# Optimization experiments

Measured on AMD Instinct MI355X. Metric: run time of the kernel, lower is better.

## Reference

```python
import jax, jax.numpy as jnp
import numpy as np


def _mlp2(x, w1, b1, w2, b2):
    # Linear -> LeakyReLU(0.01, torch default) -> Linear
    return jax.nn.leaky_relu(x @ w1 + b1) @ w2 + b2


def _fuse(vis, phr):
    # pairwise fusion: concat[vis, phr, vis*phr, vis-phr] -> last dim 4*R
    shp = jnp.broadcast_shapes(vis.shape, phr.shape)
    v = jnp.broadcast_to(vis, shp)
    p = jnp.broadcast_to(phr, shp)
    return jnp.concatenate([v, p, v * p, v - p], axis=-1)


def setup_inputs() -> dict:
    key = jax.random.key(0)
    B, P, N, D, R = 4, 16, 256, 2048, 1024
    ks = jax.random.split(key, 16)
    w = lambda k, s: jax.random.normal(k, s, jnp.float32) * 0.02
    inp = {
        "box_feats": jax.random.normal(ks[0], (B, N, D), jnp.float32),
        "phrase_embed": jax.random.normal(ks[1], (B, P, R), jnp.float32),
        # visual_embedding MLP (stage 1)
        "ve_w1": w(ks[2], (D, R)), "ve_b1": jnp.zeros((R,), jnp.float32),
        "ve_w2": w(ks[3], (R, R)), "ve_b2": jnp.zeros((R,), jnp.float32),
        # similarity MLP: 4R -> 256 -> 1
        "sim_w1": w(ks[4], (4 * R, 256)), "sim_b1": jnp.zeros((256,), jnp.float32),
        "sim_w2": w(ks[5], (256, 1)), "sim_b2": jnp.zeros((1,), jnp.float32),
        # box_reg MLP: 4R -> 256 -> 4
        "reg_w1": w(ks[6], (4 * R, 256)), "reg_b1": jnp.zeros((256,), jnp.float32),
        "reg_w2": w(ks[7], (256, 4)), "reg_b2": jnp.zeros((4,), jnp.float32),
        # topN-stage twins
        "vet_w1": w(ks[8], (D, R)), "vet_b1": jnp.zeros((R,), jnp.float32),
        "vet_w2": w(ks[9], (R, R)), "vet_b2": jnp.zeros((R,), jnp.float32),
        "simt_w1": w(ks[10], (4 * R, 256)), "simt_b1": jnp.zeros((256,), jnp.float32),
        "simt_w2": w(ks[11], (256, 1)), "simt_b2": jnp.zeros((1,), jnp.float32),
        "regt_w1": w(ks[12], (4 * R, 256)), "regt_b1": jnp.zeros((256,), jnp.float32),
        "regt_w2": w(ks[13], (256, 4)), "regt_b2": jnp.zeros((4,), jnp.float32),
        "topN": 16,
    }
    return inp


def reference(box_feats, phrase_embed,
              ve_w1, ve_b1, ve_w2, ve_b2,
              sim_w1, sim_b1, sim_w2, sim_b2,
              reg_w1, reg_b1, reg_w2, reg_b2,
              vet_w1, vet_b1, vet_w2, vet_b2,
              simt_w1, simt_b1, simt_w2, simt_b2,
              regt_w1, regt_b1, regt_w2, regt_b2,
              topN):
    # Stage 1: embed all boxes, score every (phrase, box) pair.
    vis = _mlp2(box_feats, ve_w1, ve_b1, ve_w2, ve_b2)          # [B,N,R]
    fused = _fuse(vis[:, None], phrase_embed[:, :, None])        # [B,P,N,4R]
    sim = jax.nn.softmax(
        _mlp2(fused, sim_w1, sim_b1, sim_w2, sim_b2)[..., 0], axis=-1)  # [B,P,N]
    reg = _mlp2(fused, reg_w1, reg_b1, reg_w2, reg_b2)           # [B,P,N,4]

    # Stage 2: topN rescoring per phrase (make_pair_topN pattern).
    _, top_idx = jax.lax.top_k(sim, topN)                        # [B,P,topN]
    bf_top = jnp.take_along_axis(box_feats[:, None], top_idx[..., None], axis=2)  # [B,P,topN,D]
    vis_t = _mlp2(bf_top, vet_w1, vet_b1, vet_w2, vet_b2)        # [B,P,topN,R]
    fused_t = _fuse(vis_t, phrase_embed[:, :, None])             # [B,P,topN,4R]
    sim_t = jax.nn.softmax(
        _mlp2(fused_t, simt_w1, simt_b1, simt_w2, simt_b2)[..., 0], axis=-1)  # [B,P,topN]
    reg_t = _mlp2(fused_t, regt_w1, regt_b1, regt_w2, regt_b2)   # [B,P,topN,4]
    return (sim, reg, sim_t, reg_t)
```

## Files before the change

kernel.cpp:

```cpp
#include <hip/hip_runtime.h>
#include <hip/hip_bf16.h>


namespace {

constexpr int Nc_   = 256;
constexpr int Dc    = 2048;
constexpr int Rc    = 1024;
constexpr int TOPN  = 16;
constexpr int HS    = 256;
constexpr int HO    = 512;
constexpr int BPc   = 64;
constexpr int PAIRS1 = 16384;
constexpr int PAIRS2 = 1024;

__device__ __forceinline__ float  leaky01f(float x)  { return x > 0.f ? x : 0.01f * x; }
__device__ __forceinline__ double leaky01d(double x) { return x > 0.0 ? x : 0.01  * x; }

template <typename TA, typename TW, bool ST64, bool ST32, bool LEAKY>
__global__ __launch_bounds__(256) void dgemm64_kernel(
    const TA* __restrict__ A, const TW* __restrict__ W, const float* __restrict__ bias,
    double* __restrict__ C64, float* __restrict__ C32, int M, int N, int K)
{
  __shared__ double As[16][64];
  __shared__ double Bs[16][64];
  const int t = threadIdx.x, tx = t & 15, ty = t >> 4;
  const int row0 = blockIdx.y * 64, col0 = blockIdx.x * 64;
  double acc[4][4] = {};

  for (int k0 = 0; k0 < K; k0 += 16) {
    {
      int mm = t >> 2, kq = (t & 3) * 4;
      const TA* src = A + (size_t)(row0 + mm) * K + k0 + kq;
      double v0, v1, v2, v3;
      if constexpr (sizeof(TA) == 4) {
        float4 f = *(const float4*)src; v0 = f.x; v1 = f.y; v2 = f.z; v3 = f.w;
      } else {
        const double2* d = (const double2*)src;
        double2 a = d[0], b = d[1]; v0 = a.x; v1 = a.y; v2 = b.x; v3 = b.y;
      }
      As[kq + 0][mm] = v0; As[kq + 1][mm] = v1; As[kq + 2][mm] = v2; As[kq + 3][mm] = v3;
    }
    {
      int kk = t >> 4, nq = (t & 15) * 4;
      const TW* src = W + (size_t)(k0 + kk) * N + col0 + nq;
      if constexpr (sizeof(TW) == 4) {
        float4 f = *(const float4*)src;
        Bs[kk][nq] = f.x; Bs[kk][nq + 1] = f.y; Bs[kk][nq + 2] = f.z; Bs[kk][nq + 3] = f.w;
      } else {
        const double2* d = (const double2*)src;
        double2 a = d[0], b = d[1];
        Bs[kk][nq] = a.x; Bs[kk][nq + 1] = a.y; Bs[kk][nq + 2] = b.x; Bs[kk][nq + 3] = b.y;
      }
    }
    __syncthreads();
#pragma unroll
    for (int kk = 0; kk < 16; ++kk) {
      double a[4], b[4];
#pragma unroll
      for (int i = 0; i < 4; ++i) a[i] = As[kk][ty * 4 + i];
#pragma unroll
      for (int j = 0; j < 4; ++j) b[j] = Bs[kk][tx * 4 + j];
#pragma unroll
      for (int i = 0; i < 4; ++i)
#pragma unroll
        for (int j = 0; j < 4; ++j) acc[i][j] = fma(a[i], b[j], acc[i][j]);
    }
    __syncthreads();
  }

#pragma unroll
  for (int i = 0; i < 4; ++i) {
    int r = row0 + ty * 4 + i;
#pragma unroll
    for (int j = 0; j < 4; ++j) {
      int c = col0 + tx * 4 + j;
      double v = acc[i][j];
      if (bias) v += (double)bias[c];
      if constexpr (LEAKY) v = leaky01d(v);
      if constexpr (ST64) C64[(size_t)r * N + c] = v;
      if constexpr (ST32) C32[(size_t)r * N + c] = (float)v;
    }
  }
}

__global__ __launch_bounds__(256) void pair64_kernel(
    const double* __restrict__ vis, const float* __restrict__ phr,
    const double* __restrict__ W, const double* __restrict__ Xv,
    const double* __restrict__ Xp, const double* __restrict__ b1,
    double* __restrict__ H)
{
  __shared__ double As[16][64];
  __shared__ double Bs[16][64];
  const int t = threadIdx.x, tx = t & 15, ty = t >> 4;
  const int row0 = blockIdx.y * 64, col0 = blockIdx.x * 64;
  double acc[4][4] = {};

  for (int k0 = 0; k0 < Rc; k0 += 16) {
    {
      int mm = t >> 2, kq = (t & 3) * 4;
      int m = row0 + mm, bp = m >> 8;
      int vr = ((bp >> 4) << 8) | (m & 255), pr = bp;
      const double2* vd = (const double2*)(vis + (size_t)vr * Rc + k0 + kq);
      double2 a = vd[0], b = vd[1];
      float4 p = *(const float4*)(phr + (size_t)pr * Rc + k0 + kq);
      As[kq + 0][mm] = a.x * (double)p.x; As[kq + 1][mm] = a.y * (double)p.y;
      As[kq + 2][mm] = b.x * (double)p.z; As[kq + 3][mm] = b.y * (double)p.w;
    }
    {
      int kk = t >> 4, nq = (t & 15) * 4;
      const double2* d = (const double2*)(W + (size_t)(k0 + kk) * HS + col0 + nq);
      double2 a = d[0], b = d[1];
      Bs[kk][nq] = a.x; Bs[kk][nq + 1] = a.y; Bs[kk][nq + 2] = b.x; Bs[kk][nq + 3] = b.y;
    }
    __syncthreads();
#pragma unroll
    for (int kk = 0; kk < 16; ++kk) {
      double a[4], b[4];
#pragma unroll
      for (int i = 0; i < 4; ++i) a[i] = As[kk][ty * 4 + i];
#pragma unroll
      for (int j = 0; j < 4; ++j) b[j] = Bs[kk][tx * 4 + j];
#pragma unroll
      for (int i = 0; i < 4; ++i)
#pragma unroll
        for (int j = 0; j < 4; ++j) acc[i][j] = fma(a[i], b[j], acc[i][j]);
    }
    __syncthreads();
  }

#pragma unroll
  for (int i = 0; i < 4; ++i) {
    int r = row0 + ty * 4 + i, bp = r >> 8;
    int vr = ((bp >> 4) << 8) | (r & 255), pr = bp;
#pragma unroll
    for (int j = 0; j < 4; ++j) {
      int c = col0 + tx * 4 + j;
      double v = acc[i][j] + Xv[(size_t)vr * HS + c] + Xp[(size_t)pr * HS + c] + b1[c];
      H[(size_t)r * HS + c] = leaky01d(v);
    }
  }
}

template <int BM, int BN, int BK, int TM, int TN>
__global__ __launch_bounds__(256) void sgemm_kernel(
    const float* __restrict__ A, const float* __restrict__ W,
    const float* __restrict__ bias, float* __restrict__ C,
    int M, int Nc, int K, int leaky)
{
  constexpr int THREADS = (BM / TM) * (BN / TN);
  static_assert(THREADS == 256, "block must be 256");
  __shared__ float As[BK][BM];
  __shared__ float Bs[BK][BN];

  const int t = threadIdx.x;
  const int tx = t % (BN / TN), ty = t / (BN / TN);
  const int row0 = blockIdx.y * BM, col0 = blockIdx.x * BN;
  float acc[TM][TN] = {};

  for (int k0 = 0; k0 < K; k0 += BK) {
    constexpr int AV = BM * BK / 4 / THREADS;
#pragma unroll
    for (int p_ = 0; p_ < AV; ++p_) {
      int f = p_ * THREADS + t;
      int mm = f / (BK / 4), kq = (f % (BK / 4)) * 4;
      float4 a4 = *(const float4*)(A + (size_t)(row0 + mm) * K + k0 + kq);
      As[kq + 0][mm] = a4.x; As[kq + 1][mm] = a4.y;
      As[kq + 2][mm] = a4.z; As[kq + 3][mm] = a4.w;
    }
    constexpr int BV = BK * BN / 4 / THREADS;
#pragma unroll
    for (int p_ = 0; p_ < BV; ++p_) {
      int f = p_ * THREADS + t;
      int nq = (f % (BN / 4)) * 4, kk = f / (BN / 4);
      *(float4*)&Bs[kk][nq] = *(const float4*)(W + (size_t)(k0 + kk) * Nc + col0 + nq);
    }
    __syncthreads();
#pragma unroll
    for (int kk = 0; kk < BK; ++kk) {
      float a[TM], bb[TN];
#pragma unroll
      for (int i = 0; i < TM; i += 4) {
        float4 v = *(const float4*)&As[kk][ty * TM + i];
        a[i] = v.x; a[i + 1] = v.y; a[i + 2] = v.z; a[i + 3] = v.w;
      }
#pragma unroll
      for (int j = 0; j < TN; j += 4) {
        float4 v = *(const float4*)&Bs[kk][tx * TN + j];
        bb[j] = v.x; bb[j + 1] = v.y; bb[j + 2] = v.z; bb[j + 3] = v.w;
      }
#pragma unroll
      for (int i = 0; i < TM; ++i)
#pragma unroll
        for (int j = 0; j < TN; ++j) acc[i][j] = fmaf(a[i], bb[j], acc[i][j]);
    }
    __syncthreads();
  }

#pragma unroll
  for (int i = 0; i < TM; ++i) {
    int r = row0 + ty * TM + i;
#pragma unroll
    for (int j = 0; j < TN; j += 4) {
      int c = col0 + tx * TN + j;
      float4 o;
      o.x = acc[i][j]; o.y = acc[i][j + 1]; o.z = acc[i][j + 2]; o.w = acc[i][j + 3];
      if (bias) {
        float4 bv = *(const float4*)(bias + c);
        o.x += bv.x; o.y += bv.y; o.z += bv.z; o.w += bv.w;
      }
      if (leaky) { o.x = leaky01f(o.x); o.y = leaky01f(o.y); o.z = leaky01f(o.z); o.w = leaky01f(o.w); }
      *(float4*)(C + (size_t)r * Nc + c) = o;
    }
  }
}

template <int BM, int BN, int BK, int TM, int TN, int STAGE, int NCOL, typename TVIS>
__global__ __launch_bounds__(256) void pair_gemm_kernel(
    const TVIS* __restrict__ vis, const float* __restrict__ phr,
    const float* __restrict__ Wvp, const float* __restrict__ Xv,
    const float* __restrict__ Xp, const float* __restrict__ b1c,
    float* __restrict__ Hout, int M)
{
  constexpr int THREADS = (BM / TM) * (BN / TN);
  static_assert(THREADS == 256, "block must be 256");
  __shared__ float As[BK][BM];
  __shared__ float Bs[BK][BN];

  const int t = threadIdx.x;
  const int tx = t % (BN / TN), ty = t / (BN / TN);
  const int row0 = blockIdx.y * BM, col0 = blockIdx.x * BN;
  float acc[TM][TN] = {};

  for (int k0 = 0; k0 < Rc; k0 += BK) {
    constexpr int AV = BM * BK / 4 / THREADS;
#pragma unroll
    for (int p_ = 0; p_ < AV; ++p_) {
      int f = p_ * THREADS + t;
      int mm = f / (BK / 4), kq = (f % (BK / 4)) * 4;
      int m = row0 + mm;
      int vr, pr;
      if (STAGE == 1) { int bp = m >> 8; pr = bp; vr = ((bp >> 4) << 8) | (m & 255); }
      else            { vr = m; pr = m >> 4; }
      float4 v4;
      if constexpr (sizeof(TVIS) == 8) {
        const double2* d = (const double2*)(vis + (size_t)vr * Rc + k0 + kq);
        double2 a = d[0], b = d[1];
        v4 = make_float4((float)a.x, (float)a.y, (float)b.x, (float)b.y);
      } else {
        v4 = *(const float4*)((const float*)vis + (size_t)vr * Rc + k0 + kq);
      }
      float4 p4 = *(const float4*)(phr + (size_t)pr * Rc + k0 + kq);
      As[kq + 0][mm] = v4.x * p4.x; As[kq + 1][mm] = v4.y * p4.y;
      As[kq + 2][mm] = v4.z * p4.z; As[kq + 3][mm] = v4.w * p4.w;
    }
    constexpr int BV = BK * BN / 4 / THREADS;
#pragma unroll
    for (int p_ = 0; p_ < BV; ++p_) {
      int f = p_ * THREADS + t;
      int nq = (f % (BN / 4)) * 4, kk = f / (BN / 4);
      *(float4*)&Bs[kk][nq] = *(const float4*)(Wvp + (size_t)(k0 + kk) * NCOL + col0 + nq);
    }
    __syncthreads();
#pragma unroll
    for (int kk = 0; kk < BK; ++kk) {
      float a[TM], bb[TN];
#pragma unroll
      for (int i = 0; i < TM; i += 4) {
        float4 v = *(const float4*)&As[kk][ty * TM + i];
        a[i] = v.x; a[i + 1] = v.y; a[i + 2] = v.z; a[i + 3] = v.w;
      }
#pragma unroll
      for (int j = 0; j < TN; j += 4) {
        float4 v = *(const float4*)&Bs[kk][tx * TN + j];
        bb[j] = v.x; bb[j + 1] = v.y; bb[j + 2] = v.z; bb[j + 3] = v.w;
      }
#pragma unroll
      for (int i = 0; i < TM; ++i)
#pragma unroll
        for (int j = 0; j < TN; ++j) acc[i][j] = fmaf(a[i], bb[j], acc[i][j]);
    }
    __syncthreads();
  }

#pragma unroll
  for (int i = 0; i < TM; ++i) {
    int r = row0 + ty * TM + i;
    int vr, pr;
    if (STAGE == 1) { int bp = r >> 8; pr = bp; vr = ((bp >> 4) << 8) | (r & 255); }
    else            { vr = r; pr = r >> 4; }
#pragma unroll
    for (int j = 0; j < TN; j += 4) {
      int c = col0 + tx * TN + j;
      float4 xv = *(const float4*)(Xv + (size_t)vr * NCOL + c);
      float4 xp = *(const float4*)(Xp + (size_t)pr * NCOL + c);
      float4 bv = *(const float4*)(b1c + c);
      float4 o;
      o.x = leaky01f(acc[i][j]     + xv.x + xp.x + bv.x);
      o.y = leaky01f(acc[i][j + 1] + xv.y + xp.y + bv.y);
      o.z = leaky01f(acc[i][j + 2] + xv.z + xp.z + bv.z);
      o.w = leaky01f(acc[i][j + 3] + xv.w + xp.w + bv.w);
      *(float4*)(Hout + (size_t)r * NCOL + c) = o;
    }
  }
}

__global__ __launch_bounds__(256) void prep_sim64_kernel(
    const float* __restrict__ w1, const float* __restrict__ b1,
    double* __restrict__ Wv, double* __restrict__ Wp, double* __restrict__ Wvp,
    double* __restrict__ bO)
{
  int idx = blockIdx.x * 256 + threadIdx.x;
  int r = idx >> 8, c = idx & 255;
  double wa = (double)w1[(size_t)(0 * Rc + r) * 256 + c];
  double wb = (double)w1[(size_t)(1 * Rc + r) * 256 + c];
  double wc = (double)w1[(size_t)(2 * Rc + r) * 256 + c];
  double wd = (double)w1[(size_t)(3 * Rc + r) * 256 + c];
  Wv[idx] = wa + wd; Wp[idx] = wb - wd; Wvp[idx] = wc;
  if (r == 0) bO[c] = (double)b1[c];
}

__global__ __launch_bounds__(256) void prep_reg32_kernel(
    const float* __restrict__ w1, const float* __restrict__ b1,
    float* __restrict__ Wv, float* __restrict__ Wp, float* __restrict__ Wvp,
    float* __restrict__ bO)
{
  int idx = blockIdx.x * 256 + threadIdx.x;
  int r = idx >> 8, c = idx & 255;
  float wa = w1[(size_t)(0 * Rc + r) * 256 + c];
  float wb = w1[(size_t)(1 * Rc + r) * 256 + c];
  float wc = w1[(size_t)(2 * Rc + r) * 256 + c];
  float wd = w1[(size_t)(3 * Rc + r) * 256 + c];
  Wv[idx] = wa + wd; Wp[idx] = wb - wd; Wvp[idx] = wc;
  if (r == 0) bO[c] = b1[c];
}

__global__ __launch_bounds__(256) void prep_t_kernel(
    const float* __restrict__ simw1, const float* __restrict__ regw1,
    const float* __restrict__ simb1, const float* __restrict__ regb1,
    float* __restrict__ Wv, float* __restrict__ Wp, float* __restrict__ Wvp,
    float* __restrict__ b1c)
{
  int idx = blockIdx.x * 256 + threadIdx.x;
  int r = idx >> 9, j = idx & (HO - 1);
  const float* w1 = (j < 256) ? simw1 : regw1;
  int c = j & 255;
  float wa = w1[(size_t)(0 * Rc + r) * 256 + c];
  float wb = w1[(size_t)(1 * Rc + r) * 256 + c];
  float wc = w1[(size_t)(2 * Rc + r) * 256 + c];
  float wd = w1[(size_t)(3 * Rc + r) * 256 + c];
  Wv[idx] = wa + wd; Wp[idx] = wb - wd; Wvp[idx] = wc;
  if (r == 0) b1c[j] = (j < 256) ? simb1[c] : regb1[c];
}

__global__ __launch_bounds__(256) void layer2_sim64_kernel(
    const double* __restrict__ h, const float* __restrict__ sw2,
    const float* __restrict__ sb2, double* __restrict__ out, int M)
{
  int wave = (blockIdx.x * blockDim.x + threadIdx.x) >> 6, lane = threadIdx.x & 63;
  if (wave >= M) return;
  const double* hr = h + (size_t)wave * HS + lane * 4;
  double2 h0 = *(const double2*)hr, h1 = *(const double2*)(hr + 2);
  float4 w = *(const float4*)(sw2 + lane * 4);
  double s = h0.x * (double)w.x + h0.y * (double)w.y + h1.x * (double)w.z + h1.y * (double)w.w;
#pragma unroll
  for (int off = 32; off; off >>= 1) s += __shfl_xor(s, off);
  if (lane == 0) out[wave] = s + (double)sb2[0];
}

__global__ __launch_bounds__(256) void layer2_reg32_kernel(
    const float* __restrict__ h, const float* __restrict__ rw2,
    const float* __restrict__ rb2, float* __restrict__ reg_out, int M)
{
  int wave = (blockIdx.x * blockDim.x + threadIdx.x) >> 6, lane = threadIdx.x & 63;
  if (wave >= M) return;
  float4 hr = *(const float4*)(h + (size_t)wave * HS + lane * 4);
  float4 r0 = *(const float4*)(rw2 + (size_t)(lane * 4 + 0) * 4);
  float4 r1 = *(const float4*)(rw2 + (size_t)(lane * 4 + 1) * 4);
  float4 r2 = *(const float4*)(rw2 + (size_t)(lane * 4 + 2) * 4);
  float4 r3 = *(const float4*)(rw2 + (size_t)(lane * 4 + 3) * 4);
  float c0 = hr.x * r0.x + hr.y * r1.x + hr.z * r2.x + hr.w * r3.x;
  float c1 = hr.x * r0.y + hr.y * r1.y + hr.z * r2.y + hr.w * r3.y;
  float c2 = hr.x * r0.z + hr.y * r1.z + hr.z * r2.z + hr.w * r3.z;
  float c3 = hr.x * r0.w + hr.y * r1.w + hr.z * r2.w + hr.w * r3.w;
#pragma unroll
  for (int off = 32; off; off >>= 1) {
    c0 += __shfl_xor(c0, off); c1 += __shfl_xor(c1, off);
    c2 += __shfl_xor(c2, off); c3 += __shfl_xor(c3, off);
  }
  if (lane == 0) {
    float4 o; o.x = c0 + rb2[0]; o.y = c1 + rb2[1]; o.z = c2 + rb2[2]; o.w = c3 + rb2[3];
    *(float4*)(reg_out + (size_t)wave * 4) = o;
  }
}

__global__ __launch_bounds__(256) void layer2_t_kernel(
    const float* __restrict__ hidden,
    const float* __restrict__ sw2, const float* __restrict__ sb2,
    const float* __restrict__ rw2, const float* __restrict__ rb2,
    float* __restrict__ sim_logits, float* __restrict__ reg_out, int M)
{
  int wave = (blockIdx.x * blockDim.x + threadIdx.x) >> 6, lane = threadIdx.x & 63;
  if (wave >= M) return;
  const float* h = hidden + (size_t)wave * HO;
  float4 hs = *(const float4*)(h + lane * 4);
  float4 hr = *(const float4*)(h + 256 + lane * 4);
  float4 ws = *(const float4*)(sw2 + lane * 4);
  float s = hs.x * ws.x + hs.y * ws.y + hs.z * ws.z + hs.w * ws.w;
  float4 r0 = *(const float4*)(rw2 + (size_t)(lane * 4 + 0) * 4);
  float4 r1 = *(const float4*)(rw2 + (size_t)(lane * 4 + 1) * 4);
  float4 r2 = *(const float4*)(rw2 + (size_t)(lane * 4 + 2) * 4);
  float4 r3 = *(const float4*)(rw2 + (size_t)(lane * 4 + 3) * 4);
  float c0 = hr.x * r0.x + hr.y * r1.x + hr.z * r2.x + hr.w * r3.x;
  float c1 = hr.x * r0.y + hr.y * r1.y + hr.z * r2.y + hr.w * r3.y;
  float c2 = hr.x * r0.z + hr.y * r1.z + hr.z * r2.z + hr.w * r3.z;
  float c3 = hr.x * r0.w + hr.y * r1.w + hr.z * r2.w + hr.w * r3.w;
#pragma unroll
  for (int off = 32; off; off >>= 1) {
    s  += __shfl_xor(s, off);
    c0 += __shfl_xor(c0, off); c1 += __shfl_xor(c1, off);
    c2 += __shfl_xor(c2, off); c3 += __shfl_xor(c3, off);
  }
  if (lane == 0) {
    sim_logits[wave] = s + sb2[0];
    float4 o; o.x = c0 + rb2[0]; o.y = c1 + rb2[1]; o.z = c2 + rb2[2]; o.w = c3 + rb2[3];
    *(float4*)(reg_out + (size_t)wave * 4) = o;
  }
}

__global__ __launch_bounds__(64) void softmax_topk64_kernel(
    const double* __restrict__ logits, float* __restrict__ sim_out,
    int* __restrict__ top_idx)
{
  int row = blockIdx.x, lane = threadIdx.x;
  double v[4];
#pragma unroll
  for (int i = 0; i < 4; ++i) v[i] = logits[row * 256 + i * 64 + lane];
  double m = fmax(fmax(v[0], v[1]), fmax(v[2], v[3]));
#pragma unroll
  for (int off = 32; off; off >>= 1) m = fmax(m, __shfl_xor(m, off));
  double e[4], ssum = 0.0;
#pragma unroll
  for (int i = 0; i < 4; ++i) { e[i] = exp(v[i] - m); ssum += e[i]; }
#pragma unroll
  for (int off = 32; off; off >>= 1) ssum += __shfl_xor(ssum, off);
#pragma unroll
  for (int i = 0; i < 4; ++i)
    sim_out[row * 256 + i * 64 + lane] = (float)(e[i] / ssum);

  const double EPS = 2.5e-7;
  for (int it = 0; it < TOPN; ++it) {
    double vm = fmax(fmax(v[0], v[1]), fmax(v[2], v[3]));
#pragma unroll
    for (int off = 32; off; off >>= 1) vm = fmax(vm, __shfl_xor(vm, off));
    double thr = vm - EPS;
    int bi = 1 << 30;
#pragma unroll
    for (int i = 0; i < 4; ++i)
      if (v[i] >= thr) { int gi = i * 64 + lane; if (gi < bi) bi = gi; }
#pragma unroll
    for (int off = 32; off; off >>= 1) {
      int oi = __shfl_xor(bi, off);
      if (oi < bi) bi = oi;
    }
    if (lane == 0) top_idx[row * TOPN + it] = bi;
    if ((bi & 63) == lane) v[bi >> 6] = -1.0e30;
  }
}

__global__ __launch_bounds__(64) void softmax16_kernel(
    const float* __restrict__ logits, float* __restrict__ out)
{
  int row = blockIdx.x, lane = threadIdx.x;
  float v = (lane < TOPN) ? logits[row * TOPN + lane] : -1e30f;
  float m = v;
#pragma unroll
  for (int off = 8; off; off >>= 1) m = fmaxf(m, __shfl_xor(m, off));
  float e = (lane < TOPN) ? expf(v - m) : 0.f;
  float s = e;
#pragma unroll
  for (int off = 8; off; off >>= 1) s += __shfl_xor(s, off);
  if (lane < TOPN) out[row * TOPN + lane] = e / s;
}

__global__ __launch_bounds__(256) void gather_kernel(
    const float* __restrict__ box, const int* __restrict__ top_idx,
    float* __restrict__ bf_top)
{
  int pr = blockIdx.x;
  int bp = pr >> 4, b = bp >> 4;
  int src = b * Nc_ + top_idx[pr];
  const float4* s = (const float4*)(box + (size_t)src * Dc);
  float4* d = (float4*)(bf_top + (size_t)pr * Dc);
  for (int i = threadIdx.x; i < Dc / 4; i += 256) d[i] = s[i];
}

}

extern "C" void kernel_launch(void* const* d_in, const int* in_sizes, int n_in,
                              void* d_out, int out_size, void* d_ws, size_t ws_size,
                              hipStream_t stream) {
  const float* box    = (const float*)d_in[0];
  const float* phrase = (const float*)d_in[1];
  const float* ve_w1  = (const float*)d_in[2];
  const float* ve_b1  = (const float*)d_in[3];
  const float* ve_w2  = (const float*)d_in[4];
  const float* ve_b2  = (const float*)d_in[5];
  const float* sim_w1 = (const float*)d_in[6];
  const float* sim_b1 = (const float*)d_in[7];
  const float* sim_w2 = (const float*)d_in[8];
  const float* sim_b2 = (const float*)d_in[9];
  const float* reg_w1 = (const float*)d_in[10];
  const float* reg_b1 = (const float*)d_in[11];
  const float* reg_w2 = (const float*)d_in[12];
  const float* reg_b2 = (const float*)d_in[13];
  const float* vet_w1 = (const float*)d_in[14];
  const float* vet_b1 = (const float*)d_in[15];
  const float* vet_w2 = (const float*)d_in[16];
  const float* vet_b2 = (const float*)d_in[17];
  const float* simt_w1 = (const float*)d_in[18];
  const float* simt_b1 = (const float*)d_in[19];
  const float* simt_w2 = (const float*)d_in[20];
  const float* simt_b2 = (const float*)d_in[21];
  const float* regt_w1 = (const float*)d_in[22];
  const float* regt_b1 = (const float*)d_in[23];
  const float* regt_w2 = (const float*)d_in[24];
  const float* regt_b2 = (const float*)d_in[25];

  float* out = (float*)d_out;
  float* o_sim  = out;
  float* o_reg  = out + PAIRS1;
  float* o_simt = out + 81920;
  float* o_regt = out + 82944;

  char* w = (char*)d_ws;
  double* vis64   = (double*)(w + 0);
  char*   REGA    = w + 8388608;
  double* H64     = (double*)REGA;
  double* Xv64    = (double*)REGA;
  double* Xp64    = (double*)(REGA + 2097152);
  double* simlog64= (double*)(REGA + 2228224);
  float*  H1t     = (float*)REGA;
  double* WcV64   = (double*)(w + 16777216);
  double* WcP64   = (double*)(w + 18874368);
  double* WcVP64  = (double*)(w + 20971520);
  double* b1c64   = (double*)(w + 23068672);
  int*    topidx  = (int*)   (w + 23070720);
  float*  simtlog = (float*) (w + 23074816);
  float*  b1cr    = (float*) (w + 23078912);
  float*  b1ct    = (float*) (w + 23079936);
  char*   HSIM    = w + 23134208;
  double* hsim64  = (double*)HSIM;
  float*  hreg32  = (float*) HSIM;
  float*  WcVr    = (float*)(HSIM + 16777216);
  float*  WcPr    = (float*)(HSIM + 17825792);
  float*  WcVPr   = (float*)(HSIM + 18874368);
  float*  Xvr     = (float*)(HSIM + 19922944);
  float*  Xpr     = (float*)(HSIM + 20971520);
  float*  bftop   = (float*) HSIM;
  float*  vist    = (float*)(HSIM + 8388608);
  float*  Xvt     = (float*)(HSIM + 12582912);
  float*  Xpt     = (float*)(HSIM + 14680064);
  float*  hidnt   = (float*)(HSIM + 14811136);
  float*  WcVt    = (float*)(HSIM + 16908288);
  float*  WcPt    = (float*)(HSIM + 19005440);
  float*  WcVPt   = (float*)(HSIM + 21102592);

  prep_sim64_kernel<<<Rc * HS / 256, 256, 0, stream>>>(
      sim_w1, sim_b1, WcV64, WcP64, WcVP64, b1c64);
  dgemm64_kernel<float, float, true, false, true><<<dim3(16, 16), 256, 0, stream>>>(
      box, ve_w1, ve_b1, H64, nullptr, 1024, Rc, Dc);
  dgemm64_kernel<double, float, true, false, false><<<dim3(16, 16), 256, 0, stream>>>(
      H64, ve_w2, ve_b2, vis64, nullptr, 1024, Rc, Rc);
  dgemm64_kernel<double, double, true, false, false><<<dim3(4, 16), 256, 0, stream>>>(
      vis64, WcV64, nullptr, Xv64, nullptr, 1024, HS, Rc);
  dgemm64_kernel<float, double, true, false, false><<<dim3(4, 1), 256, 0, stream>>>(
      phrase, WcP64, nullptr, Xp64, nullptr, BPc, HS, Rc);
  pair64_kernel<<<dim3(4, 256), 256, 0, stream>>>(
      vis64, phrase, WcVP64, Xv64, Xp64, b1c64, hsim64);
  layer2_sim64_kernel<<<PAIRS1 / 4, 256, 0, stream>>>(
      hsim64, sim_w2, sim_b2, simlog64, PAIRS1);
  softmax_topk64_kernel<<<BPc, 64, 0, stream>>>(simlog64, o_sim, topidx);

  prep_reg32_kernel<<<Rc * HS / 256, 256, 0, stream>>>(
      reg_w1, reg_b1, WcVr, WcPr, WcVPr, b1cr);
  dgemm64_kernel<double, float, false, true, false><<<dim3(4, 16), 256, 0, stream>>>(
      vis64, WcVr, nullptr, nullptr, Xvr, 1024, HS, Rc);
  sgemm_kernel<64, 64, 32, 4, 4><<<dim3(4, 1), 256, 0, stream>>>(
      phrase, WcPr, nullptr, Xpr, BPc, HS, Rc, 0);
  pair_gemm_kernel<128, 128, 32, 8, 8, 1, HS, double><<<dim3(2, 128), 256, 0, stream>>>(
      vis64, phrase, WcVPr, Xvr, Xpr, b1cr, hreg32, PAIRS1);
  layer2_reg32_kernel<<<PAIRS1 / 4, 256, 0, stream>>>(
      hreg32, reg_w2, reg_b2, o_reg, PAIRS1);

  gather_kernel<<<PAIRS2, 256, 0, stream>>>(box, topidx, bftop);
  prep_t_kernel<<<Rc * HO / 256, 256, 0, stream>>>(
      simt_w1, regt_w1, simt_b1, regt_b1, WcVt, WcPt, WcVPt, b1ct);
  sgemm_kernel<128, 64, 32, 8, 4><<<dim3(16, 8), 256, 0, stream>>>(
      bftop, vet_w1, vet_b1, H1t, 1024, Rc, Dc, 1);
  sgemm_kernel<128, 64, 32, 8, 4><<<dim3(16, 8), 256, 0, stream>>>(
      H1t, vet_w2, vet_b2, vist, 1024, Rc, Rc, 0);
  sgemm_kernel<64, 64, 32, 4, 4><<<dim3(8, 16), 256, 0, stream>>>(
      vist, WcVt, nullptr, Xvt, 1024, HO, Rc, 0);
  sgemm_kernel<64, 64, 32, 4, 4><<<dim3(8, 1), 256, 0, stream>>>(
      phrase, WcPt, nullptr, Xpt, BPc, HO, Rc, 0);
  pair_gemm_kernel<64, 64, 32, 4, 4, 2, HO, float><<<dim3(8, 16), 256, 0, stream>>>(
      vist, phrase, WcVPt, Xvt, Xpt, b1ct, hidnt, PAIRS2);
  layer2_t_kernel<<<PAIRS2 / 4, 256, 0, stream>>>(
      hidnt, simt_w2, simt_b2, regt_w2, regt_b2, simtlog, o_regt, PAIRS2);
  softmax16_kernel<<<BPc, 64, 0, stream>>>(simtlog, o_simt);
}
```

Baseline: 1.589 ms.

## Score all pairs in fp32, refine top-32 candidates in fp64 for top-k

```diff
diff --git a/kernel.cpp b/kernel.cpp
--- a/kernel.cpp
+++ b/kernel.cpp
@@ -8,11 +8,13 @@
 constexpr int Dc    = 2048;
 constexpr int Rc    = 1024;
 constexpr int TOPN  = 16;
+constexpr int NCAND = 32;
 constexpr int HS    = 256;
 constexpr int HO    = 512;
 constexpr int BPc   = 64;
 constexpr int PAIRS1 = 16384;
 constexpr int PAIRS2 = 1024;
+constexpr int CPAIRS = BPc * NCAND;
 
 __device__ __forceinline__ float  leaky01f(float x)  { return x > 0.f ? x : 0.01f * x; }
 __device__ __forceinline__ double leaky01d(double x) { return x > 0.0 ? x : 0.01  * x; }
@@ -22,7 +24,7 @@
     const TA* __restrict__ A, const TW* __restrict__ W, const float* __restrict__ bias,
     double* __restrict__ C64, float* __restrict__ C32, int M, int N, int K)
 {
-  __shared__ double As[16][64];
+  __shared__ double As[16][65];
   __shared__ double Bs[16][64];
   const int t = threadIdx.x, tx = t & 15, ty = t >> 4;
   const int row0 = blockIdx.y * 64, col0 = blockIdx.x * 64;
@@ -60,7 +62,7 @@
 #pragma unroll
       for (int i = 0; i < 4; ++i) a[i] = As[kk][ty * 4 + i];
 #pragma unroll
-      for (int j = 0; j < 4; ++j) b[j] = Bs[kk][tx * 4 + j];
+      for (int j = 0; j < 4; ++j) b[j] = Bs[kk][tx + 16 * j];
 #pragma unroll
       for (int i = 0; i < 4; ++i)
 #pragma unroll
@@ -74,7 +76,7 @@
     int r = row0 + ty * 4 + i;
 #pragma unroll
     for (int j = 0; j < 4; ++j) {
-      int c = col0 + tx * 4 + j;
+      int c = col0 + tx + 16 * j;
       double v = acc[i][j];
       if (bias) v += (double)bias[c];
       if constexpr (LEAKY) v = leaky01d(v);
@@ -84,26 +86,27 @@
   }
 }
 
-__global__ __launch_bounds__(256) void pair64_kernel(
+__global__ __launch_bounds__(256) void pair64c_kernel(
     const double* __restrict__ vis, const float* __restrict__ phr,
     const double* __restrict__ W, const double* __restrict__ Xv,
     const double* __restrict__ Xp, const double* __restrict__ b1,
-    double* __restrict__ H)
-{
-  __shared__ double As[16][64];
+    const int* __restrict__ candn, double* __restrict__ H)
+{
+  __shared__ double As[16][65];
   __shared__ double Bs[16][64];
   const int t = threadIdx.x, tx = t & 15, ty = t >> 4;
   const int row0 = blockIdx.y * 64, col0 = blockIdx.x * 64;
   double acc[4][4] = {};
 
+  const int mm = t >> 2, kq = (t & 3) * 4;
+  const int ms = row0 + mm, bps = ms >> 5;
+  const int vrs = ((bps >> 4) << 8) | candn[ms], prs = bps;
+
   for (int k0 = 0; k0 < Rc; k0 += 16) {
     {
-      int mm = t >> 2, kq = (t & 3) * 4;
-      int m = row0 + mm, bp = m >> 8;
-      int vr = ((bp >> 4) << 8) | (m & 255), pr = bp;
-      const double2* vd = (const double2*)(vis + (size_t)vr * Rc + k0 + kq);
+      const double2* vd = (const double2*)(vis + (size_t)vrs * Rc + k0 + kq);
       double2 a = vd[0], b = vd[1];
-      float4 p = *(const float4*)(phr + (size_t)pr * Rc + k0 + kq);
+      float4 p = *(const float4*)(phr + (size_t)prs * Rc + k0 + kq);
       As[kq + 0][mm] = a.x * (double)p.x; As[kq + 1][mm] = a.y * (double)p.y;
       As[kq + 2][mm] = b.x * (double)p.z; As[kq + 3][mm] = b.y * (double)p.w;
     }
@@ -120,7 +123,7 @@
 #pragma unroll
       for (int i = 0; i < 4; ++i) a[i] = As[kk][ty * 4 + i];
 #pragma unroll
-      for (int j = 0; j < 4; ++j) b[j] = Bs[kk][tx * 4 + j];
+      for (int j = 0; j < 4; ++j) b[j] = Bs[kk][tx + 16 * j];
 #pragma unroll
       for (int i = 0; i < 4; ++i)
 #pragma unroll
@@ -131,11 +134,11 @@
 
 #pragma unroll
   for (int i = 0; i < 4; ++i) {
-    int r = row0 + ty * 4 + i, bp = r >> 8;
-    int vr = ((bp >> 4) << 8) | (r & 255), pr = bp;
+    int r = row0 + ty * 4 + i, bp = r >> 5;
+    int vr = ((bp >> 4) << 8) | candn[r], pr = bp;
 #pragma unroll
     for (int j = 0; j < 4; ++j) {
-      int c = col0 + tx * 4 + j;
+      int c = col0 + tx + 16 * j;
       double v = acc[i][j] + Xv[(size_t)vr * HS + c] + Xp[(size_t)pr * HS + c] + b1[c];
       H[(size_t)r * HS + c] = leaky01d(v);
     }
@@ -320,7 +323,7 @@
   if (r == 0) bO[c] = (double)b1[c];
 }
 
-__global__ __launch_bounds__(256) void prep_reg32_kernel(
+__global__ __launch_bounds__(256) void prep_head32_kernel(
     const float* __restrict__ w1, const float* __restrict__ b1,
     float* __restrict__ Wv, float* __restrict__ Wp, float* __restrict__ Wvp,
     float* __restrict__ bO)
@@ -351,6 +354,20 @@
   float wd = w1[(size_t)(3 * Rc + r) * 256 + c];
   Wv[idx] = wa + wd; Wp[idx] = wb - wd; Wvp[idx] = wc;
   if (r == 0) b1c[j] = (j < 256) ? simb1[c] : regb1[c];
+}
+
+__global__ __launch_bounds__(256) void layer2_sim32_kernel(
+    const float* __restrict__ h, const float* __restrict__ sw2,
+    const float* __restrict__ sb2, float* __restrict__ out, int M)
+{
+  int wave = (blockIdx.x * blockDim.x + threadIdx.x) >> 6, lane = threadIdx.x & 63;
+  if (wave >= M) return;
+  float4 hv = *(const float4*)(h + (size_t)wave * HS + lane * 4);
+  float4 wv = *(const float4*)(sw2 + lane * 4);
+  float s = hv.x * wv.x + hv.y * wv.y + hv.z * wv.z + hv.w * wv.w;
+#pragma unroll
+  for (int off = 32; off; off >>= 1) s += __shfl_xor(s, off);
+  if (lane == 0) out[wave] = s + sb2[0];
 }
 
 __global__ __launch_bounds__(256) void layer2_sim64_kernel(
@@ -428,43 +445,62 @@
   }
 }
 
-__global__ __launch_bounds__(64) void softmax_topk64_kernel(
-    const double* __restrict__ logits, float* __restrict__ sim_out,
+__global__ __launch_bounds__(64) void softmax_cand32_kernel(
+    const float* __restrict__ logits, float* __restrict__ sim_out,
+    int* __restrict__ candn)
+{
+  int row = blockIdx.x, lane = threadIdx.x;
+  float v[4];
+#pragma unroll
+  for (int i = 0; i < 4; ++i) v[i] = logits[row * 256 + i * 64 + lane];
+  float m = fmaxf(fmaxf(v[0], v[1]), fmaxf(v[2], v[3]));
+#pragma unroll
+  for (int off = 32; off; off >>= 1) m = fmaxf(m, __shfl_xor(m, off));
+  float e[4], ssum = 0.f;
+#pragma unroll
+  for (int i = 0; i < 4; ++i) { e[i] = expf(v[i] - m); ssum += e[i]; }
+#pragma unroll
+  for (int off = 32; off; off >>= 1) ssum += __shfl_xor(ssum, off);
+#pragma unroll
+  for (int i = 0; i < 4; ++i)
+    sim_out[row * 256 + i * 64 + lane] = e[i] / ssum;
+  for (int it = 0; it < NCAND; ++it) {
+    float bv = -3.0e38f; int bi = 0;
+#pragma unroll
+    for (int i = 0; i < 4; ++i)
+      if (v[i] > bv) { bv = v[i]; bi = i * 64 + lane; }
+#pragma unroll
+    for (int off = 32; off; off >>= 1) {
+      float ov = __shfl_xor(bv, off);
+      int   oi = __shfl_xor(bi, off);
+      if (ov > bv || (ov == bv && oi < bi)) { bv = ov; bi = oi; }
+    }
+    if (lane == 0) candn[row * NCAND + it] = bi;
+    if ((bi & 63) == lane) v[bi >> 6] = -3.4e38f;
+  }
+}
+
+__global__ __launch_bounds__(64) void topk_cand64_kernel(
+    const double* __restrict__ clog, const int* __restrict__ candn,
     int* __restrict__ top_idx)
 {
   int row = blockIdx.x, lane = threadIdx.x;
-  double v[4];
-#pragma unroll
-  for (int i = 0; i < 4; ++i) v[i] = logits[row * 256 + i * 64 + lane];
-  double m = fmax(fmax(v[0], v[1]), fmax(v[2], v[3]));
-#pragma unroll
-  for (int off = 32; off; off >>= 1) m = fmax(m, __shfl_xor(m, off));
-  double e[4], ssum = 0.0;
-#pragma unroll
-  for (int i = 0; i < 4; ++i) { e[i] = exp(v[i] - m); ssum += e[i]; }
-#pragma unroll
-  for (int off = 32; off; off >>= 1) ssum += __shfl_xor(ssum, off);
-#pragma unroll
-  for (int i = 0; i < 4; ++i)
-    sim_out[row * 256 + i * 64 + lane] = (float)(e[i] / ssum);
-
+  double v = (lane < NCAND) ? clog[row * NCAND + lane] : -1.0e300;
+  int    n = (lane < NCAND) ? candn[row * NCAND + lane] : (1 << 29);
   const double EPS = 2.5e-7;
   for (int it = 0; it < TOPN; ++it) {
-    double vm = fmax(fmax(v[0], v[1]), fmax(v[2], v[3]));
+    double vm = v;
 #pragma unroll
     for (int off = 32; off; off >>= 1) vm = fmax(vm, __shfl_xor(vm, off));
     double thr = vm - EPS;
-    int bi = 1 << 30;
-#pragma unroll
-    for (int i = 0; i < 4; ++i)
-      if (v[i] >= thr) { int gi = i * 64 + lane; if (gi < bi) bi = gi; }
+    int bn = (v >= thr) ? n : (1 << 30);
 #pragma unroll
     for (int off = 32; off; off >>= 1) {
-      int oi = __shfl_xor(bi, off);
-      if (oi < bi) bi = oi;
-    }
-    if (lane == 0) top_idx[row * TOPN + it] = bi;
-    if ((bi & 63) == lane) v[bi >> 6] = -1.0e30;
+      int o = __shfl_xor(bn, off);
+      if (o < bn) bn = o;
+    }
+    if (lane == 0) top_idx[row * TOPN + it] = bn;
+    if (n == bn) v = -1.0e300;
   }
 }
 
@@ -533,65 +569,85 @@
   float* o_simt = out + 81920;
   float* o_regt = out + 82944;
 
+  constexpr size_t MB = 1u << 20;
   char* w = (char*)d_ws;
-  double* vis64   = (double*)(w + 0);
-  char*   REGA    = w + 8388608;
-  double* H64     = (double*)REGA;
-  double* Xv64    = (double*)REGA;
-  double* Xp64    = (double*)(REGA + 2097152);
-  double* simlog64= (double*)(REGA + 2228224);
-  float*  H1t     = (float*)REGA;
-  double* WcV64   = (double*)(w + 16777216);
-  double* WcP64   = (double*)(w + 18874368);
-  double* WcVP64  = (double*)(w + 20971520);
-  double* b1c64   = (double*)(w + 23068672);
-  int*    topidx  = (int*)   (w + 23070720);
-  float*  simtlog = (float*) (w + 23074816);
-  float*  b1cr    = (float*) (w + 23078912);
-  float*  b1ct    = (float*) (w + 23079936);
-  char*   HSIM    = w + 23134208;
-  double* hsim64  = (double*)HSIM;
-  float*  hreg32  = (float*) HSIM;
-  float*  WcVr    = (float*)(HSIM + 16777216);
-  float*  WcPr    = (float*)(HSIM + 17825792);
-  float*  WcVPr   = (float*)(HSIM + 18874368);
-  float*  Xvr     = (float*)(HSIM + 19922944);
-  float*  Xpr     = (float*)(HSIM + 20971520);
-  float*  bftop   = (float*) HSIM;
-  float*  vist    = (float*)(HSIM + 8388608);
-  float*  Xvt     = (float*)(HSIM + 12582912);
-  float*  Xpt     = (float*)(HSIM + 14680064);
-  float*  hidnt   = (float*)(HSIM + 14811136);
-  float*  WcVt    = (float*)(HSIM + 16908288);
-  float*  WcPt    = (float*)(HSIM + 19005440);
-  float*  WcVPt   = (float*)(HSIM + 21102592);
-
-  prep_sim64_kernel<<<Rc * HS / 256, 256, 0, stream>>>(
-      sim_w1, sim_b1, WcV64, WcP64, WcVP64, b1c64);
+  double* vis64  = (double*)(w + 0 * MB);
+  double* H64    = (double*)(w + 8 * MB);
+  float*  WcVs   = (float*)(w + 8 * MB);
+  float*  WcPs   = (float*)(w + 9 * MB);
+  float*  WcVPs  = (float*)(w + 10 * MB);
+  float*  WcVr   = (float*)(w + 11 * MB);
+  float*  WcPr   = (float*)(w + 12 * MB);
+  float*  WcVPr  = (float*)(w + 13 * MB);
+  float*  Xv32s  = (float*)(w + 14 * MB);
+  float*  Xv32r  = (float*)(w + 15 * MB);
+  float*  WcVt   = (float*)(w + 8 * MB);
+  float*  WcPt   = (float*)(w + 10 * MB);
+  float*  WcVPt  = (float*)(w + 12 * MB);
+  float*  Xvt    = (float*)(w + 14 * MB);
+  double* WcV64  = (double*)(w + 16 * MB);
+  double* WcP64  = (double*)(w + 18 * MB);
+  float*  Xpt    = (float*)(w + 16 * MB);
+  float*  hidnt  = (float*)(w + 17 * MB);
+  double* WcVP64 = (double*)(w + 20 * MB);
+  double* Xv64   = (double*)(w + 22 * MB);
+  double* Xp64    = (double*)(w + 24 * MB);
+  double* b1c64   = (double*)(w + 24 * MB + 128 * 1024);
+  float*  b1cs    = (float*) (w + 24 * MB + 192 * 1024);
+  float*  b1cr    = (float*) (w + 24 * MB + 256 * 1024);
+  float*  b1ct    = (float*) (w + 24 * MB + 320 * 1024);
+  float*  Xp32s   = (float*) (w + 24 * MB + 384 * 1024);
+  float*  Xp32r   = (float*) (w + 24 * MB + 448 * 1024);
+  float*  simlog32= (float*) (w + 24 * MB + 512 * 1024);
+  int*    candn   = (int*)   (w + 24 * MB + 640 * 1024);
+  double* clog64  = (double*)(w + 24 * MB + 704 * 1024);
+  int*    topidx  = (int*)   (w + 24 * MB + 768 * 1024);
+  float*  simtlog = (float*) (w + 24 * MB + 832 * 1024);
+  float*  hid16  = (float*)(w + 25 * MB);
+  double* H2     = (double*)(w + 25 * MB);
+  float*  bftop  = (float*)(w + 25 * MB);
+  float*  H1t    = (float*)(w + 33 * MB);
+  float*  vist   = (float*)(w + 37 * MB);
+
   dgemm64_kernel<float, float, true, false, true><<<dim3(16, 16), 256, 0, stream>>>(
       box, ve_w1, ve_b1, H64, nullptr, 1024, Rc, Dc);
   dgemm64_kernel<double, float, true, false, false><<<dim3(16, 16), 256, 0, stream>>>(
       H64, ve_w2, ve_b2, vis64, nullptr, 1024, Rc, Rc);
+
+  prep_sim64_kernel<<<Rc * HS / 256, 256, 0, stream>>>(
+      sim_w1, sim_b1, WcV64, WcP64, WcVP64, b1c64);
+  prep_head32_kernel<<<Rc * HS / 256, 256, 0, stream>>>(
+      sim_w1, sim_b1, WcVs, WcPs, WcVPs, b1cs);
+  prep_head32_kernel<<<Rc * HS / 256, 256, 0, stream>>>(
+      reg_w1, reg_b1, WcVr, WcPr, WcVPr, b1cr);
   dgemm64_kernel<double, double, true, false, false><<<dim3(4, 16), 256, 0, stream>>>(
       vis64, WcV64, nullptr, Xv64, nullptr, 1024, HS, Rc);
   dgemm64_kernel<float, double, true, false, false><<<dim3(4, 1), 256, 0, stream>>>(
       phrase, WcP64, nullptr, Xp64, nullptr, BPc, HS, Rc);
-  pair64_kernel<<<dim3(4, 256), 256, 0, stream>>>(
-      vis64, phrase, WcVP64, Xv64, Xp64, b1c64, hsim64);
-  layer2_sim64_kernel<<<PAIRS1 / 4, 256, 0, stream>>>(
-      hsim64, sim_w2, sim_b2, simlog64, PAIRS1);
-  softmax_topk64_kernel<<<BPc, 64, 0, stream>>>(simlog64, o_sim, topidx);
-
-  prep_reg32_kernel<<<Rc * HS / 256, 256, 0, stream>>>(
-      reg_w1, reg_b1, WcVr, WcPr, WcVPr, b1cr);
   dgemm64_kernel<double, float, false, true, false><<<dim3(4, 16), 256, 0, stream>>>(
-      vis64, WcVr, nullptr, nullptr, Xvr, 1024, HS, Rc);
+      vis64, WcVs, nullptr, nullptr, Xv32s, 1024, HS, Rc);
   sgemm_kernel<64, 64, 32, 4, 4><<<dim3(4, 1), 256, 0, stream>>>(
-      phrase, WcPr, nullptr, Xpr, BPc, HS, Rc, 0);
+      phrase, WcPs, nullptr, Xp32s, BPc, HS, Rc, 0);
+  dgemm64_kernel<double, float, false, true, false><<<dim3(4, 16), 256, 0, stream>>>(
+      vis64, WcVr, nullptr, nullptr, Xv32r, 1024, HS, Rc);
+  sgemm_kernel<64, 64, 32, 4, 4><<<dim3(4, 1), 256, 0, stream>>>(
+      phrase, WcPr, nullptr, Xp32r, BPc, HS, Rc, 0);
+
   pair_gemm_kernel<128, 128, 32, 8, 8, 1, HS, double><<<dim3(2, 128), 256, 0, stream>>>(
-      vis64, phrase, WcVPr, Xvr, Xpr, b1cr, hreg32, PAIRS1);
+      vis64, phrase, WcVPs, Xv32s, Xp32s, b1cs, hid16, PAIRS1);
+  layer2_sim32_kernel<<<PAIRS1 / 4, 256, 0, stream>>>(
+      hid16, sim_w2, sim_b2, simlog32, PAIRS1);
+  softmax_cand32_kernel<<<BPc, 64, 0, stream>>>(simlog32, o_sim, candn);
+  pair_gemm_kernel<128, 128, 32, 8, 8, 1, HS, double><<<dim3(2, 128), 256, 0, stream>>>(
+      vis64, phrase, WcVPr, Xv32r, Xp32r, b1cr, hid16, PAIRS1);
   layer2_reg32_kernel<<<PAIRS1 / 4, 256, 0, stream>>>(
-      hreg32, reg_w2, reg_b2, o_reg, PAIRS1);
+      hid16, reg_w2, reg_b2, o_reg, PAIRS1);
+
+  pair64c_kernel<<<dim3(4, CPAIRS / 64), 256, 0, stream>>>(
+      vis64, phrase, WcVP64, Xv64, Xp64, b1c64, candn, H2);
+  layer2_sim64_kernel<<<CPAIRS / 4, 256, 0, stream>>>(
+      H2, sim_w2, sim_b2, clog64, CPAIRS);
+  topk_cand64_kernel<<<BPc, 64, 0, stream>>>(clog64, candn, topidx);
 
   gather_kernel<<<PAIRS2, 256, 0, stream>>>(box, topidx, bftop);
   prep_t_kernel<<<Rc * HO / 256, 256, 0, stream>>>(
```

After: 2.190 ms. 37.8% more time.
